# Optimization experiments

Hardware: AMD Instinct MI355X
Metric: run time of the kernel (lower is better)

The kernel has to match this reference:

```python
import jax, jax.numpy as jnp
import numpy as np

RANK = 8
A_SHAPE = (64, 128)   # (a1, a2)
B_SHAPE = (16, 32)    # (b1, b2)
BATCH = 16384


def setup_inputs() -> dict:
    key = jax.random.key(0)
    k1, k2, k3, k4, k5 = jax.random.split(key, 5)
    a1, a2 = A_SHAPE
    b1, b2 = B_SHAPE
    x = jax.random.normal(k1, (BATCH, a1 * b1), dtype=jnp.float32)
    # xavier-uniform style init for a and b (as in nn.init.xavier_uniform_)
    lim_a = float(np.sqrt(6.0 / (a1 + a2)))
    lim_b = float(np.sqrt(6.0 / (b1 + b2)))
    a = jax.random.uniform(k2, (RANK, a1, a2), minval=-lim_a, maxval=lim_a, dtype=jnp.float32)
    b = jax.random.uniform(k3, (RANK, b1, b2), minval=-lim_b, maxval=lim_b, dtype=jnp.float32)
    s = jax.random.normal(k4, (a1, a2), dtype=jnp.float32)          # structured-sparse mask
    bias = jax.random.normal(k5, (a2 * b2,), dtype=jnp.float32)     # bias_shape[1:] = (a2*b2,)
    return {"x": x, "a": a, "b": b, "s": s, "bias": bias}


def reference(x, a, b, s, bias):
    # structured-sparse elementwise mask on a
    a_eff = s[None, :, :] * a                          # (rank, a1, a2)
    r, a1, a2 = a_eff.shape
    _, b1, b2 = b.shape
    # w = sum_r kron(a_eff[r], b[r]) : (a1*b1, a2*b2)
    w = jnp.einsum('rij,rkl->ikjl', a_eff, b).reshape(a1 * b1, a2 * b2)
    out = x @ w                                        # (batch, a2*b2)
    return out + bias[None, :]
```

## Files before the change

### kernel.cpp

```cpp
#include <hip/hip_runtime.h>
#include <hip/hip_bf16.h>

typedef short bf16x8 __attribute__((ext_vector_type(8)));
typedef float f32x4 __attribute__((ext_vector_type(4)));

static constexpr int M_DIM = 16384;
static constexpr int N_DIM = 4096;
static constexpr int K_DIM = 1024;

static constexpr int CVT_BLOCKS = (M_DIM * K_DIM / 8) / 256;
static constexpr int WT_BLOCKS  = N_DIM;

__device__ __forceinline__ unsigned short f2bf(float f) {
  union { float f; unsigned u; } v; v.f = f;
  unsigned r = v.u + 0x7FFFu + ((v.u >> 16) & 1u);
  return (unsigned short)(r >> 16);
}

__global__ __launch_bounds__(256) void prep_kernel(
    const float* __restrict__ x, const float* __restrict__ a,
    const float* __restrict__ b, const float* __restrict__ s,
    unsigned short* __restrict__ xb, unsigned short* __restrict__ wT) {
  __shared__ float as_eff[8][64];
  __shared__ float bl[8][16];
  const int tid = threadIdx.x;

  if (blockIdx.x < CVT_BLOCKS) {
    const int i = (blockIdx.x * 256 + tid) * 2;
    float4 v0 = reinterpret_cast<const float4*>(x)[i];
    float4 v1 = reinterpret_cast<const float4*>(x)[i + 1];
    ushort4 o0, o1;
    o0.x = f2bf(v0.x); o0.y = f2bf(v0.y); o0.z = f2bf(v0.z); o0.w = f2bf(v0.w);
    o1.x = f2bf(v1.x); o1.y = f2bf(v1.y); o1.z = f2bf(v1.z); o1.w = f2bf(v1.w);
    reinterpret_cast<ushort4*>(xb)[i] = o0;
    reinterpret_cast<ushort4*>(xb)[i + 1] = o1;
    return;
  }

  const int n = blockIdx.x - CVT_BLOCKS;
  const int j = n >> 5, l = n & 31;

#pragma unroll
  for (int t = tid; t < 512; t += 256) {
    const int r = t >> 6, i = t & 63;
    as_eff[r][i] = a[(r * 64 + i) * 128 + j] * s[i * 128 + j];
  }
  if (tid < 128) {
    const int r = tid >> 4, kk = tid & 15;
    bl[r][kk] = b[(r * 16 + kk) * 32 + l];
  }
  __syncthreads();

  const int i = tid >> 2;
  const int kk0 = (tid & 3) * 4;
  float o[4] = {0.f, 0.f, 0.f, 0.f};
#pragma unroll
  for (int r = 0; r < 8; ++r) {
    const float av = as_eff[r][i];
#pragma unroll
    for (int q = 0; q < 4; ++q)
      o[q] += av * bl[r][kk0 + q];
  }
  ushort4 w4;
  w4.x = f2bf(o[0]); w4.y = f2bf(o[1]); w4.z = f2bf(o[2]); w4.w = f2bf(o[3]);
  *reinterpret_cast<ushort4*>(&wT[(size_t)n * K_DIM + tid * 4]) = w4;
}

#define PH_BARRIER __builtin_amdgcn_s_barrier()
#define SCHED0     __builtin_amdgcn_sched_barrier(0)
#define WAITV(N)   do { asm volatile("s_waitcnt vmcnt(" #N ")" ::: "memory"); SCHED0; } while (0)
#define WAITL(N)   do { asm volatile("s_waitcnt lgkmcnt(" #N ")" ::: "memory"); SCHED0; } while (0)

__device__ __forceinline__ void quad_mfma(f32x4 (&acc)[8][4], const bf16x8 (&aH)[4][2],
                                          const bf16x8 (&bH)[2][2], int mbase, int nbase) {
  __builtin_amdgcn_s_setprio(1);
#pragma unroll
  for (int ks = 0; ks < 2; ++ks)
#pragma unroll
    for (int mi = 0; mi < 4; ++mi)
#pragma unroll
      for (int ni = 0; ni < 2; ++ni)
        acc[mbase + mi][nbase + ni] = __builtin_amdgcn_mfma_f32_16x16x32_bf16(
            aH[mi][ks], bH[ni][ks], acc[mbase + mi][nbase + ni], 0, 0, 0);
  __builtin_amdgcn_s_setprio(0);
}

__global__ __launch_bounds__(512, 2) void gemm8_kernel(
    const unsigned short* __restrict__ A, const unsigned short* __restrict__ BT,
    const float* __restrict__ bias, float* __restrict__ C) {
  __shared__ __align__(16) unsigned short Al[2][16384];
  __shared__ __align__(16) unsigned short Bl[2][16384];

  const int tid  = threadIdx.x;
  const int lane = tid & 63;
  const int wave = tid >> 6;
  const int wm = wave >> 2;
  const int wn = wave & 3;
  const int wr = wm * 128;
  const int wc = wn * 64;
  const int frow = lane & 15;
  const int kg = lane >> 4;
  const int swz0 = (kg * 16) ^ ((lane & 7) << 4);
  const int swz1 = (64 + kg * 16) ^ ((lane & 7) << 4);

  int bid = blockIdx.x;
  int gid = bid >> 4, lid = bid & 15;
  gid = ((gid & 7) << 3) | (gid >> 3);
  const int bm = (gid >> 2) * 4 + (lid >> 2);
  const int bn = (gid & 3) * 4 + (lid & 3);
  const int brow = bm * 256, bcol = bn * 256;

  const unsigned short* Abase = A + (size_t)brow * K_DIM;
  const unsigned short* Bbase = BT + (size_t)bcol * K_DIM;

  const int srow = tid >> 3;
  const int scol = ((((tid & 7) << 4) ^ ((srow & 7) << 4)) >> 1);
  const int ldsu = __builtin_amdgcn_readfirstlane(wave * 512);

#define STG(dst, base, q, k0) __builtin_amdgcn_global_load_lds( \
    (const __attribute__((address_space(1))) void*)((base) + (size_t)((q)*64 + srow) * K_DIM + (k0) + scol), \
    (__attribute__((address_space(3))) void*)((dst) + (q)*4096 + ldsu), 16, 0, 0)

#define STG4(dst, base, k0) do { STG(dst, base, 0, k0); STG(dst, base, 1, k0); \
                                 STG(dst, base, 2, k0); STG(dst, base, 3, k0); } while (0)

#define LOAD_AH(P, h) { _Pragma("unroll") for (int mi = 0; mi < 4; ++mi) { \
    const char* p_ = (const char*)(P) + (wr + frow + ((h)*4 + mi) * 16) * 128; \
    aF[mi][0] = *(const bf16x8*)(p_ + swz0); aF[mi][1] = *(const bf16x8*)(p_ + swz1); } }

#define LOAD_BH(P, h, dst) { _Pragma("unroll") for (int ni = 0; ni < 2; ++ni) { \
    const char* p_ = (const char*)(P) + (wc + frow + ((h)*2 + ni) * 16) * 128; \
    dst[ni][0] = *(const bf16x8*)(p_ + swz0); dst[ni][1] = *(const bf16x8*)(p_ + swz1); } }

  f32x4 acc[8][4] = {};
  bf16x8 aF[4][2], b0[2][2], b1[2][2];

  STG4(Bl[0], Bbase, 0);
  STG4(Al[0], Abase, 0);
  STG4(Bl[1], Bbase, 64);
  WAITV(4);
  PH_BARRIER;

#define TILE(PA, PB, SA, SB, VM) \
  LOAD_AH(PA, 0); SCHED0; \
  LOAD_BH(PB, 0, b0); SCHED0; \
  LOAD_BH(PB, 1, b1); SCHED0; \
  SA; \
  WAITL(4); \
  quad_mfma(acc, aF, b0, 0, 0); \
  WAITL(0); \
  quad_mfma(acc, aF, b1, 0, 2); \
  LOAD_AH(PA, 1); SCHED0; \
  WAITL(0); \
  quad_mfma(acc, aF, b1, 4, 2); \
  PH_BARRIER; \
  SB; \
  quad_mfma(acc, aF, b0, 4, 0); \
  VM; \
  PH_BARRIER;

  int k = 0;
#pragma unroll 1
  for (int i = 0; i < 7; ++i) {
    TILE(Al[0], Bl[0], STG4(Al[1], Abase, k + 64), STG4(Bl[0], Bbase, k + 128), WAITV(4));
    TILE(Al[1], Bl[1], STG4(Al[0], Abase, k + 128), STG4(Bl[1], Bbase, k + 192), WAITV(4));
    k += 128;
  }
  TILE(Al[0], Bl[0], STG4(Al[1], Abase, k + 64), (void)0, WAITV(0));
  TILE(Al[1], Bl[1], (void)0, (void)0, WAITV(0));

  __syncthreads();
  float* T = (float*)&Al[0][0];
  float* Tw = T + wave * (16 * 68);
  const int col4 = lane & 15;
  const int rsel = lane >> 4;
  float4 bv = *(const float4*)&bias[bcol + wc + col4 * 4];

#pragma unroll
  for (int mi = 0; mi < 8; ++mi) {
#pragma unroll
    for (int ni = 0; ni < 4; ++ni)
#pragma unroll
      for (int r = 0; r < 4; ++r)
        Tw[(kg * 4 + r) * 68 + ni * 16 + frow] = acc[mi][ni][r];
    WAITL(0);
#pragma unroll
    for (int rr = 0; rr < 4; ++rr) {
      float4 v = *(float4*)&Tw[(rr * 4 + rsel) * 68 + col4 * 4];
      v.x += bv.x; v.y += bv.y; v.z += bv.z; v.w += bv.w;
      *(float4*)&C[(size_t)(brow + wr + mi * 16 + rr * 4 + rsel) * N_DIM + bcol + wc + col4 * 4] = v;
    }
    WAITL(0);
  }
}

extern "C" void kernel_launch(void* const* d_in, const int* in_sizes, int n_in,
                              void* d_out, int out_size, void* d_ws, size_t ws_size,
                              hipStream_t stream) {
  const float* x    = (const float*)d_in[0];
  const float* a    = (const float*)d_in[1];
  const float* b    = (const float*)d_in[2];
  const float* s    = (const float*)d_in[3];
  const float* bias = (const float*)d_in[4];
  float* out = (float*)d_out;

  unsigned short* xb = (unsigned short*)d_ws;
  unsigned short* wT = (unsigned short*)((char*)d_ws + (size_t)M_DIM * K_DIM * 2);

  prep_kernel<<<CVT_BLOCKS + WT_BLOCKS, 256, 0, stream>>>(x, a, b, s, xb, wT);
  gemm8_kernel<<<(M_DIM / 256) * (N_DIM / 256), 512, 0, stream>>>(xb, wT, bias, out);
}
```

Baseline: 186.2 us.

## Triple-buffer B tiles with one barrier per K step and batch weight build

The GEMM main loop now rotates through three B shared-memory buffers and two A buffers. This drops one of the two workgroup barriers per K tile and lets the B prefetch run two tiles ahead. The Kronecker weight-build part of the prep kernel now uses 128 blocks: each loads all of b into shared memory and computes 32 output columns, instead of one block per output column. The extra B buffer raises LDS use to about 160KB per block, and the prep path has far fewer blocks, which could underfill the GPU.

```diff
diff --git a/kernel.cpp b/kernel.cpp
--- a/kernel.cpp
+++ b/kernel.cpp
@@ -9,7 +9,7 @@
 static constexpr int K_DIM = 1024;
 
 static constexpr int CVT_BLOCKS = (M_DIM * K_DIM / 8) / 256;
-static constexpr int WT_BLOCKS  = N_DIM;
+static constexpr int WT_BLOCKS  = 128;
 
 __device__ __forceinline__ unsigned short f2bf(float f) {
   union { float f; unsigned u; } v; v.f = f;
@@ -21,8 +21,6 @@
     const float* __restrict__ x, const float* __restrict__ a,
     const float* __restrict__ b, const float* __restrict__ s,
     unsigned short* __restrict__ xb, unsigned short* __restrict__ wT) {
-  __shared__ float as_eff[8][64];
-  __shared__ float bl[8][16];
   const int tid = threadIdx.x;
 
   if (blockIdx.x < CVT_BLOCKS) {
@@ -37,34 +35,40 @@
     return;
   }
 
-  const int n = blockIdx.x - CVT_BLOCKS;
-  const int j = n >> 5, l = n & 31;
-
+  __shared__ float as_eff[8][64];
+  __shared__ float bsh[8][16][32];
+  const int j = blockIdx.x - CVT_BLOCKS;
+
+#pragma unroll
+  for (int t = tid; t < 4096; t += 256)
+    ((float*)bsh)[t] = b[t];
 #pragma unroll
   for (int t = tid; t < 512; t += 256) {
     const int r = t >> 6, i = t & 63;
     as_eff[r][i] = a[(r * 64 + i) * 128 + j] * s[i * 128 + j];
   }
-  if (tid < 128) {
-    const int r = tid >> 4, kk = tid & 15;
-    bl[r][kk] = b[(r * 16 + kk) * 32 + l];
-  }
   __syncthreads();
 
   const int i = tid >> 2;
   const int kk0 = (tid & 3) * 4;
-  float o[4] = {0.f, 0.f, 0.f, 0.f};
-#pragma unroll
-  for (int r = 0; r < 8; ++r) {
-    const float av = as_eff[r][i];
-#pragma unroll
-    for (int q = 0; q < 4; ++q)
-      o[q] += av * bl[r][kk0 + q];
-  }
-  ushort4 w4;
-  w4.x = f2bf(o[0]); w4.y = f2bf(o[1]); w4.z = f2bf(o[2]); w4.w = f2bf(o[3]);
-  *reinterpret_cast<ushort4*>(&wT[(size_t)n * K_DIM + tid * 4]) = w4;
-}
+  float av[8];
+#pragma unroll
+  for (int r = 0; r < 8; ++r) av[r] = as_eff[r][i];
+
+#pragma unroll 4
+  for (int l = 0; l < 32; ++l) {
+    float o[4] = {0.f, 0.f, 0.f, 0.f};
+#pragma unroll
+    for (int r = 0; r < 8; ++r)
+#pragma unroll
+      for (int q = 0; q < 4; ++q)
+        o[q] += av[r] * bsh[r][kk0 + q][l];
+    ushort4 w4;
+    w4.x = f2bf(o[0]); w4.y = f2bf(o[1]); w4.z = f2bf(o[2]); w4.w = f2bf(o[3]);
+    *reinterpret_cast<ushort4*>(&wT[(size_t)(j * 32 + l) * K_DIM + tid * 4]) = w4;
+  }
+}
+
 
 #define PH_BARRIER __builtin_amdgcn_s_barrier()
 #define SCHED0     __builtin_amdgcn_sched_barrier(0)
@@ -89,7 +93,7 @@
     const unsigned short* __restrict__ A, const unsigned short* __restrict__ BT,
     const float* __restrict__ bias, float* __restrict__ C) {
   __shared__ __align__(16) unsigned short Al[2][16384];
-  __shared__ __align__(16) unsigned short Bl[2][16384];
+  __shared__ __align__(16) unsigned short Bl[3][16384];
 
   const int tid  = threadIdx.x;
   const int lane = tid & 63;
@@ -141,33 +145,31 @@
   WAITV(4);
   PH_BARRIER;
 
-#define TILE(PA, PB, SA, SB, VM) \
-  LOAD_AH(PA, 0); SCHED0; \
-  LOAD_BH(PB, 0, b0); SCHED0; \
-  LOAD_BH(PB, 1, b1); SCHED0; \
-  SA; \
-  WAITL(4); \
-  quad_mfma(acc, aF, b0, 0, 0); \
-  WAITL(0); \
-  quad_mfma(acc, aF, b1, 0, 2); \
-  LOAD_AH(PA, 1); SCHED0; \
-  WAITL(0); \
-  quad_mfma(acc, aF, b1, 4, 2); \
-  PH_BARRIER; \
-  SB; \
-  quad_mfma(acc, aF, b0, 4, 0); \
-  VM; \
-  PH_BARRIER;
-
-  int k = 0;
+  unsigned short* a_rd = &Al[0][0]; unsigned short* a_st = &Al[1][0];
+  unsigned short* b_rd = &Bl[0][0]; unsigned short* b_nx = &Bl[1][0];
+  unsigned short* b_st = &Bl[2][0];
+
 #pragma unroll 1
-  for (int i = 0; i < 7; ++i) {
-    TILE(Al[0], Bl[0], STG4(Al[1], Abase, k + 64), STG4(Bl[0], Bbase, k + 128), WAITV(4));
-    TILE(Al[1], Bl[1], STG4(Al[0], Abase, k + 128), STG4(Bl[1], Bbase, k + 192), WAITV(4));
-    k += 128;
-  }
-  TILE(Al[0], Bl[0], STG4(Al[1], Abase, k + 64), (void)0, WAITV(0));
-  TILE(Al[1], Bl[1], (void)0, (void)0, WAITV(0));
+  for (int t = 0; t < 16; ++t) {
+    const int k = t * 64;
+    LOAD_AH(a_rd, 0); SCHED0;
+    LOAD_BH(b_rd, 0, b0); SCHED0;
+    LOAD_BH(b_rd, 1, b1); SCHED0;
+    if (t < 15) STG4(a_st, Abase, k + 64);
+    if (t < 14) STG4(b_st, Bbase, k + 128);
+    WAITL(4);
+    quad_mfma(acc, aF, b0, 0, 0);
+    WAITL(0);
+    quad_mfma(acc, aF, b1, 0, 2);
+    LOAD_AH(a_rd, 1); SCHED0;
+    WAITL(0);
+    quad_mfma(acc, aF, b1, 4, 2);
+    quad_mfma(acc, aF, b0, 4, 0);
+    if (t < 14) { WAITV(4); } else { WAITV(0); }
+    PH_BARRIER;
+    unsigned short* ta = a_rd; a_rd = a_st; a_st = ta;
+    unsigned short* tb = b_rd; b_rd = b_nx; b_nx = b_st; b_st = tb;
+  }
 
   __syncthreads();
   float* T = (float*)&Al[0][0];
```

After: 195.7 us. 1.05x slower.

## Prepack weights in MFMA fragment layout and load B directly into registers

Applied to the files above, without the earlier changes.

The prep kernel now writes the Kronecker weight matrix in a fragment-packed layout that matches the MFMA B operand. The GEMM then loads B straight from global memory into registers instead of staging it through LDS. This halves LDS usage and removes the LDS reads and barriers for B, and the K loop becomes a simpler single-tile double-buffered pipeline for A. The trade-off is that the two waves sharing the same columns each fetch B from global memory, so they depend on L2 bandwidth and latency hiding through the vmcnt waits.

```diff
diff --git a/kernel.cpp b/kernel.cpp
--- a/kernel.cpp
+++ b/kernel.cpp
@@ -63,33 +63,24 @@
   }
   ushort4 w4;
   w4.x = f2bf(o[0]); w4.y = f2bf(o[1]); w4.z = f2bf(o[2]); w4.w = f2bf(o[3]);
-  *reinterpret_cast<ushort4*>(&wT[(size_t)n * K_DIM + tid * 4]) = w4;
-}
+  const int n16 = n >> 4, frow = n & 15;
+  const int ks = tid >> 3;
+  const int kg = (tid >> 1) & 3;
+  const int j0 = (tid & 1) * 4;
+  const size_t flat = ((size_t)(n16 * 32 + ks) << 9) + (size_t)(kg * 16 + frow) * 8 + j0;
+  *reinterpret_cast<ushort4*>(&wT[flat]) = w4;
+}
+
 
 #define PH_BARRIER __builtin_amdgcn_s_barrier()
 #define SCHED0     __builtin_amdgcn_sched_barrier(0)
 #define WAITV(N)   do { asm volatile("s_waitcnt vmcnt(" #N ")" ::: "memory"); SCHED0; } while (0)
 #define WAITL(N)   do { asm volatile("s_waitcnt lgkmcnt(" #N ")" ::: "memory"); SCHED0; } while (0)
 
-__device__ __forceinline__ void quad_mfma(f32x4 (&acc)[8][4], const bf16x8 (&aH)[4][2],
-                                          const bf16x8 (&bH)[2][2], int mbase, int nbase) {
-  __builtin_amdgcn_s_setprio(1);
-#pragma unroll
-  for (int ks = 0; ks < 2; ++ks)
-#pragma unroll
-    for (int mi = 0; mi < 4; ++mi)
-#pragma unroll
-      for (int ni = 0; ni < 2; ++ni)
-        acc[mbase + mi][nbase + ni] = __builtin_amdgcn_mfma_f32_16x16x32_bf16(
-            aH[mi][ks], bH[ni][ks], acc[mbase + mi][nbase + ni], 0, 0, 0);
-  __builtin_amdgcn_s_setprio(0);
-}
-
-__global__ __launch_bounds__(512, 2) void gemm8_kernel(
+__global__ __launch_bounds__(512, 2) void gemm_kernel(
     const unsigned short* __restrict__ A, const unsigned short* __restrict__ BT,
     const float* __restrict__ bias, float* __restrict__ C) {
   __shared__ __align__(16) unsigned short Al[2][16384];
-  __shared__ __align__(16) unsigned short Bl[2][16384];
 
   const int tid  = threadIdx.x;
   const int lane = tid & 63;
@@ -111,63 +102,66 @@
   const int brow = bm * 256, bcol = bn * 256;
 
   const unsigned short* Abase = A + (size_t)brow * K_DIM;
-  const unsigned short* Bbase = BT + (size_t)bcol * K_DIM;
+  const int n160 = (bcol + wc) >> 4;
 
   const int srow = tid >> 3;
   const int scol = ((((tid & 7) << 4) ^ ((srow & 7) << 4)) >> 1);
   const int ldsu = __builtin_amdgcn_readfirstlane(wave * 512);
 
-#define STG(dst, base, q, k0) __builtin_amdgcn_global_load_lds( \
-    (const __attribute__((address_space(1))) void*)((base) + (size_t)((q)*64 + srow) * K_DIM + (k0) + scol), \
+#define STG(dst, q, k0) __builtin_amdgcn_global_load_lds( \
+    (const __attribute__((address_space(1))) void*)(Abase + (size_t)((q)*64 + srow) * K_DIM + (k0) + scol), \
     (__attribute__((address_space(3))) void*)((dst) + (q)*4096 + ldsu), 16, 0, 0)
 
-#define STG4(dst, base, k0) do { STG(dst, base, 0, k0); STG(dst, base, 1, k0); \
-                                 STG(dst, base, 2, k0); STG(dst, base, 3, k0); } while (0)
+#define STGA(dst, k0) do { STG(dst, 0, k0); STG(dst, 1, k0); \
+                           STG(dst, 2, k0); STG(dst, 3, k0); SCHED0; } while (0)
+
+#define LDB(dst, t2) { _Pragma("unroll") for (int ni = 0; ni < 4; ++ni) { \
+    _Pragma("unroll") for (int sl = 0; sl < 2; ++sl) \
+      dst[ni][sl] = *(const bf16x8*)(BT + (((size_t)(n160 + ni) * 32 + (t2)*2 + sl) << 9) + lane * 8); } \
+    SCHED0; }
 
 #define LOAD_AH(P, h) { _Pragma("unroll") for (int mi = 0; mi < 4; ++mi) { \
     const char* p_ = (const char*)(P) + (wr + frow + ((h)*4 + mi) * 16) * 128; \
-    aF[mi][0] = *(const bf16x8*)(p_ + swz0); aF[mi][1] = *(const bf16x8*)(p_ + swz1); } }
-
-#define LOAD_BH(P, h, dst) { _Pragma("unroll") for (int ni = 0; ni < 2; ++ni) { \
-    const char* p_ = (const char*)(P) + (wc + frow + ((h)*2 + ni) * 16) * 128; \
-    dst[ni][0] = *(const bf16x8*)(p_ + swz0); dst[ni][1] = *(const bf16x8*)(p_ + swz1); } }
+    aF[mi][0] = *(const bf16x8*)(p_ + swz0); aF[mi][1] = *(const bf16x8*)(p_ + swz1); } SCHED0; }
+
+#define MFMA32(mbase, bC) do { __builtin_amdgcn_s_setprio(1); \
+    _Pragma("unroll") for (int sl = 0; sl < 2; ++sl) \
+    _Pragma("unroll") for (int mi = 0; mi < 4; ++mi) \
+    _Pragma("unroll") for (int ni = 0; ni < 4; ++ni) \
+      acc[(mbase)+mi][ni] = __builtin_amdgcn_mfma_f32_16x16x32_bf16( \
+          aF[mi][sl], bC[ni][sl], acc[(mbase)+mi][ni], 0, 0, 0); \
+    __builtin_amdgcn_s_setprio(0); } while (0)
 
   f32x4 acc[8][4] = {};
-  bf16x8 aF[4][2], b0[2][2], b1[2][2];
-
-  STG4(Bl[0], Bbase, 0);
-  STG4(Al[0], Abase, 0);
-  STG4(Bl[1], Bbase, 64);
-  WAITV(4);
+  bf16x8 aF[4][2], bE[4][2], bO[4][2];
+
+  STGA(Al[0], 0);
+  LDB(bE, 0);
+  WAITV(8);
   PH_BARRIER;
 
-#define TILE(PA, PB, SA, SB, VM) \
-  LOAD_AH(PA, 0); SCHED0; \
-  LOAD_BH(PB, 0, b0); SCHED0; \
-  LOAD_BH(PB, 1, b1); SCHED0; \
-  SA; \
-  WAITL(4); \
-  quad_mfma(acc, aF, b0, 0, 0); \
-  WAITL(0); \
-  quad_mfma(acc, aF, b1, 0, 2); \
-  LOAD_AH(PA, 1); SCHED0; \
-  WAITL(0); \
-  quad_mfma(acc, aF, b1, 4, 2); \
-  PH_BARRIER; \
-  SB; \
-  quad_mfma(acc, aF, b0, 4, 0); \
-  VM; \
-  PH_BARRIER;
-
-  int k = 0;
+  unsigned short* a_rd = &Al[0][0]; unsigned short* a_st = &Al[1][0];
+
+#define TILE_BODY(t, bC, bN) { \
+    const int k_ = (t) * 64; \
+    if ((t) < 15) { STGA(a_st, k_ + 64); LDB(bN, (t) + 1); } \
+    LOAD_AH(a_rd, 0); \
+    if ((t) < 15) { WAITV(12); } else { WAITV(0); } \
+    WAITL(0); \
+    MFMA32(0, bC); \
+    LOAD_AH(a_rd, 1); \
+    WAITL(0); \
+    MFMA32(4, bC); \
+    if ((t) < 15) WAITV(8); \
+    PH_BARRIER; \
+    unsigned short* tp_ = a_rd; a_rd = a_st; a_st = tp_; }
+
 #pragma unroll 1
-  for (int i = 0; i < 7; ++i) {
-    TILE(Al[0], Bl[0], STG4(Al[1], Abase, k + 64), STG4(Bl[0], Bbase, k + 128), WAITV(4));
-    TILE(Al[1], Bl[1], STG4(Al[0], Abase, k + 128), STG4(Bl[1], Bbase, k + 192), WAITV(4));
-    k += 128;
-  }
-  TILE(Al[0], Bl[0], STG4(Al[1], Abase, k + 64), (void)0, WAITV(0));
-  TILE(Al[1], Bl[1], (void)0, (void)0, WAITV(0));
+  for (int i = 0; i < 8; ++i) {
+    const int t0 = i * 2;
+    TILE_BODY(t0,     bE, bO);
+    TILE_BODY(t0 + 1, bO, bE);
+  }
 
   __syncthreads();
   float* T = (float*)&Al[0][0];
@@ -208,5 +202,5 @@
   unsigned short* wT = (unsigned short*)((char*)d_ws + (size_t)M_DIM * K_DIM * 2);
 
   prep_kernel<<<CVT_BLOCKS + WT_BLOCKS, 256, 0, stream>>>(x, a, b, s, xb, wT);
-  gemm8_kernel<<<(M_DIM / 256) * (N_DIM / 256), 512, 0, stream>>>(xb, wT, bias, out);
-}
+  gemm_kernel<<<(M_DIM / 256) * (N_DIM / 256), 512, 0, stream>>>(xb, wT, bias, out);
+}
```

New measurement: 203.0 us. 9.0% more time.

## Make GEMM persistent over four column tiles and prefetch next tile during epilogue

Applied to the files above, without the earlier changes.

The GEMM grid shrinks from 1024 to 256 blocks, and each block loops over four consecutive 256-column output tiles that share the same A row panel. The first K-slices for the next tile are issued before the current tile's epilogue, so the C writes overlap with loading. The epilogue scratch moves to Al[1] with a 64-float stride in place of 68, which avoids clobbering the prefetched buffers but may add LDS bank conflicts. The swizzled block-to-tile mapping that aided L2 reuse is dropped, and 256 blocks leave fewer workgroups than the device can hold at once.

```diff
diff --git a/kernel.cpp b/kernel.cpp
--- a/kernel.cpp
+++ b/kernel.cpp
@@ -66,6 +66,7 @@
   *reinterpret_cast<ushort4*>(&wT[(size_t)n * K_DIM + tid * 4]) = w4;
 }
 
+
 #define PH_BARRIER __builtin_amdgcn_s_barrier()
 #define SCHED0     __builtin_amdgcn_sched_barrier(0)
 #define WAITV(N)   do { asm volatile("s_waitcnt vmcnt(" #N ")" ::: "memory"); SCHED0; } while (0)
@@ -85,7 +86,7 @@
   __builtin_amdgcn_s_setprio(0);
 }
 
-__global__ __launch_bounds__(512, 2) void gemm8_kernel(
+__global__ __launch_bounds__(512, 2) void gemm_kernel(
     const unsigned short* __restrict__ A, const unsigned short* __restrict__ BT,
     const float* __restrict__ bias, float* __restrict__ C) {
   __shared__ __align__(16) unsigned short Al[2][16384];
@@ -103,15 +104,12 @@
   const int swz0 = (kg * 16) ^ ((lane & 7) << 4);
   const int swz1 = (64 + kg * 16) ^ ((lane & 7) << 4);
 
-  int bid = blockIdx.x;
-  int gid = bid >> 4, lid = bid & 15;
-  gid = ((gid & 7) << 3) | (gid >> 3);
-  const int bm = (gid >> 2) * 4 + (lid >> 2);
-  const int bn = (gid & 3) * 4 + (lid & 3);
-  const int brow = bm * 256, bcol = bn * 256;
+  const int p = blockIdx.x;
+  const int bm = p & 63;
+  const int bng = p >> 6;
+  const int brow = bm * 256;
 
   const unsigned short* Abase = A + (size_t)brow * K_DIM;
-  const unsigned short* Bbase = BT + (size_t)bcol * K_DIM;
 
   const int srow = tid >> 3;
   const int scol = ((((tid & 7) << 4) ^ ((srow & 7) << 4)) >> 1);
@@ -131,15 +129,6 @@
 #define LOAD_BH(P, h, dst) { _Pragma("unroll") for (int ni = 0; ni < 2; ++ni) { \
     const char* p_ = (const char*)(P) + (wc + frow + ((h)*2 + ni) * 16) * 128; \
     dst[ni][0] = *(const bf16x8*)(p_ + swz0); dst[ni][1] = *(const bf16x8*)(p_ + swz1); } }
-
-  f32x4 acc[8][4] = {};
-  bf16x8 aF[4][2], b0[2][2], b1[2][2];
-
-  STG4(Bl[0], Bbase, 0);
-  STG4(Al[0], Abase, 0);
-  STG4(Bl[1], Bbase, 64);
-  WAITV(4);
-  PH_BARRIER;
 
 #define TILE(PA, PB, SA, SB, VM) \
   LOAD_AH(PA, 0); SCHED0; \
@@ -159,38 +148,62 @@
   VM; \
   PH_BARRIER;
 
-  int k = 0;
-#pragma unroll 1
-  for (int i = 0; i < 7; ++i) {
-    TILE(Al[0], Bl[0], STG4(Al[1], Abase, k + 64), STG4(Bl[0], Bbase, k + 128), WAITV(4));
-    TILE(Al[1], Bl[1], STG4(Al[0], Abase, k + 128), STG4(Bl[1], Bbase, k + 192), WAITV(4));
-    k += 128;
-  }
-  TILE(Al[0], Bl[0], STG4(Al[1], Abase, k + 64), (void)0, WAITV(0));
-  TILE(Al[1], Bl[1], (void)0, (void)0, WAITV(0));
-
-  __syncthreads();
-  float* T = (float*)&Al[0][0];
-  float* Tw = T + wave * (16 * 68);
   const int col4 = lane & 15;
   const int rsel = lane >> 4;
-  float4 bv = *(const float4*)&bias[bcol + wc + col4 * 4];
-
-#pragma unroll
-  for (int mi = 0; mi < 8; ++mi) {
-#pragma unroll
-    for (int ni = 0; ni < 4; ++ni)
-#pragma unroll
-      for (int r = 0; r < 4; ++r)
-        Tw[(kg * 4 + r) * 68 + ni * 16 + frow] = acc[mi][ni][r];
-    WAITL(0);
-#pragma unroll
-    for (int rr = 0; rr < 4; ++rr) {
-      float4 v = *(float4*)&Tw[(rr * 4 + rsel) * 68 + col4 * 4];
-      v.x += bv.x; v.y += bv.y; v.z += bv.z; v.w += bv.w;
-      *(float4*)&C[(size_t)(brow + wr + mi * 16 + rr * 4 + rsel) * N_DIM + bcol + wc + col4 * 4] = v;
-    }
-    WAITL(0);
+  float* Tw = (float*)&Al[1][0] + wave * 1024;
+
+#pragma unroll 1
+  for (int jj = 0; jj < 4; ++jj) {
+    const int bcol = (bng * 4 + jj) * 256;
+    const unsigned short* Bbase = BT + (size_t)bcol * K_DIM;
+
+    if (jj == 0) {
+      STG4(Bl[0], Bbase, 0);
+      STG4(Al[0], Abase, 0);
+      STG4(Bl[1], Bbase, 64);
+      WAITV(4);
+    } else {
+      WAITV(36);
+    }
+    PH_BARRIER;
+
+    f32x4 acc[8][4] = {};
+    bf16x8 aF[4][2], b0[2][2], b1[2][2];
+
+    int k = 0;
+#pragma unroll 1
+    for (int i = 0; i < 7; ++i) {
+      TILE(Al[0], Bl[0], STG4(Al[1], Abase, k + 64), STG4(Bl[0], Bbase, k + 128), WAITV(4));
+      TILE(Al[1], Bl[1], STG4(Al[0], Abase, k + 128), STG4(Bl[1], Bbase, k + 192), WAITV(4));
+      k += 128;
+    }
+    TILE(Al[0], Bl[0], STG4(Al[1], Abase, k + 64), (void)0, WAITV(0));
+    TILE(Al[1], Bl[1], (void)0, (void)0, WAITV(0));
+
+    if (jj < 3) {
+      const unsigned short* BbaseN = BT + (size_t)((bng * 4 + jj + 1) * 256) * K_DIM;
+      STG4(Bl[0], BbaseN, 0);
+      STG4(Al[0], Abase, 0);
+      STG4(Bl[1], BbaseN, 64);
+    }
+
+    float4 bv = *(const float4*)&bias[bcol + wc + col4 * 4];
+#pragma unroll
+    for (int mi = 0; mi < 8; ++mi) {
+#pragma unroll
+      for (int ni = 0; ni < 4; ++ni)
+#pragma unroll
+        for (int r = 0; r < 4; ++r)
+          Tw[(kg * 4 + r) * 64 + ni * 16 + frow] = acc[mi][ni][r];
+      WAITL(0);
+#pragma unroll
+      for (int rr = 0; rr < 4; ++rr) {
+        float4 v = *(float4*)&Tw[(rr * 4 + rsel) * 64 + col4 * 4];
+        v.x += bv.x; v.y += bv.y; v.z += bv.z; v.w += bv.w;
+        *(float4*)&C[(size_t)(brow + wr + mi * 16 + rr * 4 + rsel) * N_DIM + bcol + wc + col4 * 4] = v;
+      }
+      WAITL(0);
+    }
   }
 }
 
@@ -208,5 +221,5 @@
   unsigned short* wT = (unsigned short*)((char*)d_ws + (size_t)M_DIM * K_DIM * 2);
 
   prep_kernel<<<CVT_BLOCKS + WT_BLOCKS, 256, 0, stream>>>(x, a, b, s, xb, wT);
-  gemm8_kernel<<<(M_DIM / 256) * (N_DIM / 256), 512, 0, stream>>>(xb, wT, bias, out);
-}
+  gemm_kernel<<<256, 512, 0, stream>>>(xb, wT, bias, out);
+}
```

Measured after the change: 186.5 us. About the same (+0.1%).
